# Performance work log

Hardware: AMD Instinct MI355X
Metric: run time of the kernel (lower is better)

## Reference

```python
import jax, jax.numpy as jnp
import numpy as np

B, CIN, H, W = 8, 64, 56, 56
COUT, K, HEADS, PAD = 64, 7, 8, 3


def hswish(x):
    return x * jnp.clip(x + 3.0, 0.0, 6.0) / 6.0


def grouped_1x1(x, w):
    # x: (B, Cin, H, W); w: (G, Cout_g, Cin_g)  -> (B, Cout, H, W)
    b, cin, h, wd = x.shape
    g = w.shape[0]
    xg = x.reshape(b, g, cin // g, h, wd)
    y = jnp.einsum('bgihw,goi->bgohw', xg, w)
    return y.reshape(b, g * w.shape[1], h, wd)


def unfold2d(x, k, h_out, w_out):
    # x: (B, C, Hp, Wp) -> (B, C, h_out, w_out, k, k), stride 1
    cols = [x[:, :, i:i + h_out, j:j + w_out] for i in range(k) for j in range(k)]
    s = jnp.stack(cols, axis=-1)  # (B,C,h,w,k*k) in (kh,kw) row-major order
    return s.reshape(*s.shape[:-1], k, k)


def setup_inputs() -> dict:
    key = jax.random.key(0)
    k1, k2, k3, k4, k5, k6 = jax.random.split(key, 6)
    cin_g, cout_g = CIN // HEADS, COUT // HEADS
    fan_out = cout_g  # 1x1 kernel, kaiming fan_out per group
    std = float(np.sqrt(2.0 / fan_out))
    return {
        'x': jax.random.normal(k1, (B, CIN, H, W), dtype=jnp.float32),
        'wq': jax.random.normal(k2, (HEADS, cout_g, cin_g), dtype=jnp.float32) * std,
        'wk': jax.random.normal(k3, (HEADS, cout_g, cin_g), dtype=jnp.float32) * std,
        'wv': jax.random.normal(k4, (HEADS, cout_g, cin_g), dtype=jnp.float32) * std,
        'rel_h': jax.random.normal(k5, (COUT // 2, 1, 1, K, 1), dtype=jnp.float32),
        'rel_w': jax.random.normal(k6, (COUT // 2, 1, 1, 1, K), dtype=jnp.float32),
    }


def reference(x, wq, wk, wv, rel_h, rel_w):
    b, _, h, w = x.shape
    heads = wq.shape[0]
    d = COUT // heads
    padded = jnp.pad(x, ((0, 0), (0, 0), (PAD, PAD), (PAD, PAD)))
    q = grouped_1x1(x, wq)                       # (B, Cout, H, W)
    k_full = grouped_1x1(padded, wk)             # (B, Cout, Hp, Wp)
    v_full = hswish(grouped_1x1(padded, wv))
    kp = unfold2d(k_full, K, h, w)               # (B, Cout, H, W, K, K)
    vp = unfold2d(v_full, K, h, w)
    kh, kw_ = kp[:, :COUT // 2], kp[:, COUT // 2:]
    kp = jnp.concatenate((kh + rel_h, kw_ + rel_w), axis=1)
    kp = kp.reshape(b, heads, d, h, w, K * K)
    vp = vp.reshape(b, heads, d, h, w, K * K)
    qh = q.reshape(b, heads, d, h, w, 1)
    # NOTE: faithful to original bug: sqrt(heads // out_channels) == 0.0
    scale = float(np.sqrt(heads // COUT))
    logits = (qh * kp).sum(axis=2, keepdims=True) * scale  # (B,heads,1,H,W,K*K)
    attn = jax.nn.softmax(logits, axis=-1)
    out = (attn * vp).sum(axis=-1)               # (B, heads, d, H, W)
    return out.reshape(b, heads * d, h, w)
```

## Files before the change

### kernel.cpp

```cpp
#include <hip/hip_runtime.h>


namespace {
constexpr int Bn = 8, CINn = 64, Hn = 56, Wn = 56;
constexpr int HEADSn = 8;
constexpr int PADn = 3;
constexpr int TH = 4;
constexpr int NTILES = Hn / TH;
constexpr int PH = TH + 6;
constexpr int PW = Wn + 6;
constexpr int RS = 80;
constexpr int THREADS = 256;
constexpr int NRUNS = Wn / 2;
}

__device__ __forceinline__ int sx(int x) { return x + (x >> 2); }
__device__ __forceinline__ float4 f4add(float4 a, float4 b) {
    return make_float4(a.x + b.x, a.y + b.y, a.z + b.z, a.w + b.w);
}
__device__ __forceinline__ float4 f4sub(float4 a, float4 b) {
    return make_float4(a.x - b.x, a.y - b.y, a.z - b.z, a.w - b.w);
}

__global__ __launch_bounds__(THREADS) void saconv_r2(
    const float* __restrict__ x, const float* __restrict__ wv,
    float* __restrict__ out)
{
    __shared__ float  wvs[64];
    __shared__ float4 vt[2 * PH * RS];
    __shared__ float4 vs[2 * TH * RS];

    const int bid  = blockIdx.x;
    const int tile = bid % NTILES;
    const int g    = (bid / NTILES) % HEADSn;
    const int b    = bid / (NTILES * HEADSn);
    const int h0   = tile * TH;
    const int tid  = threadIdx.x;

    if (tid < 64) wvs[tid] = wv[g * 64 + tid];
    __syncthreads();

    const float* __restrict__ xg = x + (size_t)(b * CINn + g * 8) * (Hn * Wn);

    for (int p = tid; p < PH * PW; p += THREADS) {
        const int py = p / PW;
        const int px = p - py * PW;
        const int y  = h0 + py - PADn;
        const int xx = px - PADn;
        float4 v0 = make_float4(0.f, 0.f, 0.f, 0.f);
        float4 v1 = v0;
        if ((unsigned)y < (unsigned)Hn && (unsigned)xx < (unsigned)Wn) {
            float in[8];
            #pragma unroll
            for (int i = 0; i < 8; ++i)
                in[i] = xg[i * (Hn * Wn) + y * Wn + xx];
            float a[8];
            #pragma unroll
            for (int o = 0; o < 8; ++o) {
                float s = 0.f;
                #pragma unroll
                for (int i = 0; i < 8; ++i)
                    s = fmaf(wvs[o * 8 + i], in[i], s);
                float t = fminf(fmaxf(s + 3.f, 0.f), 6.f);
                a[o] = s * t * (1.f / 6.f);
            }
            v0 = make_float4(a[0], a[1], a[2], a[3]);
            v1 = make_float4(a[4], a[5], a[6], a[7]);
        }
        vt[(0 * PH + py) * RS + sx(px)] = v0;
        vt[(1 * PH + py) * RS + sx(px)] = v1;
    }
    __syncthreads();

    if (tid < 2 * PW * 2) {
        const int g4 = tid & 1;
        const int r  = tid >> 1;
        const int xx = r % PW;
        const int yh = r / PW;
        const int y0 = 2 * yh;
        float4 rv[8];
        #pragma unroll
        for (int j = 0; j < 8; ++j)
            rv[j] = vt[(g4 * PH + y0 + j) * RS + sx(xx)];
        float4 s = rv[0];
        #pragma unroll
        for (int j = 1; j < 7; ++j) s = f4add(s, rv[j]);
        vs[(g4 * TH + y0) * RS + sx(xx)] = s;
        s = f4add(s, f4sub(rv[7], rv[0]));
        vs[(g4 * TH + y0 + 1) * RS + sx(xx)] = s;
    }
    __syncthreads();

    if (tid < TH * NRUNS * 2) {
        const int g4  = tid & 1;
        const int r   = tid >> 1;
        const int run = r % NRUNS;
        const int y   = r / NRUNS;
        const int x0  = run * 2;
        float4 rv[8];
        #pragma unroll
        for (int j = 0; j < 8; ++j)
            rv[j] = vs[(g4 * TH + y) * RS + sx(x0 + j)];
        float4 s0 = rv[0];
        #pragma unroll
        for (int j = 1; j < 7; ++j) s0 = f4add(s0, rv[j]);
        float4 s1 = f4add(s0, f4sub(rv[7], rv[0]));
        const float inv = 1.f / 49.f;
        float* ob = out + ((size_t)(b * CINn + g * 8 + g4 * 4) * Hn + (h0 + y)) * Wn + x0;
        const int plane = Hn * Wn;
        float2 st;
        st.x = s0.x * inv; st.y = s1.x * inv; *(float2*)(ob + 0 * plane) = st;
        st.x = s0.y * inv; st.y = s1.y * inv; *(float2*)(ob + 1 * plane) = st;
        st.x = s0.z * inv; st.y = s1.z * inv; *(float2*)(ob + 2 * plane) = st;
        st.x = s0.w * inv; st.y = s1.w * inv; *(float2*)(ob + 3 * plane) = st;
    }
}

extern "C" void kernel_launch(void* const* d_in, const int* in_sizes, int n_in,
                              void* d_out, int out_size, void* d_ws, size_t ws_size,
                              hipStream_t stream) {
    const float* x  = (const float*)d_in[0];
    const float* wv = (const float*)d_in[3];
    float* out = (float*)d_out;

    dim3 grid(Bn * HEADSn * NTILES);
    saconv_r2<<<grid, THREADS, 0, stream>>>(x, wv, out);
}
```

Measured before the change: 11.75 us.

## Fuse vertical box sum into register pass and halve tile height

Each thread now owns one padded column and one 4-channel half-head. It computes the hswish value projection for 8 input rows and accumulates the two vertical 7-row sums directly in registers, so the intermediate value tile in shared memory and one barrier stage go away. Weights are loaded into registers instead of shared memory. Tile height drops to 2 rows with 128 threads, which doubles the block count. The trade-off is more redundant recomputation and re-reading of input rows, since 8 rows are processed for every 2 output rows.

Result: slower. 13.30 us (+13.3%).

```diff
diff --git a/kernel.cpp b/kernel.cpp
--- a/kernel.cpp
+++ b/kernel.cpp
@@ -5,12 +5,11 @@
 constexpr int Bn = 8, CINn = 64, Hn = 56, Wn = 56;
 constexpr int HEADSn = 8;
 constexpr int PADn = 3;
-constexpr int TH = 4;
+constexpr int TH = 2;
 constexpr int NTILES = Hn / TH;
-constexpr int PH = TH + 6;
 constexpr int PW = Wn + 6;
-constexpr int RS = 80;
-constexpr int THREADS = 256;
+constexpr int RSH = 78;
+constexpr int THREADS = 128;
 constexpr int NRUNS = Wn / 2;
 }
 
@@ -22,13 +21,11 @@
     return make_float4(a.x - b.x, a.y - b.y, a.z - b.z, a.w - b.w);
 }
 
-__global__ __launch_bounds__(THREADS) void saconv_r2(
+__global__ __launch_bounds__(THREADS) void saconv_r4(
     const float* __restrict__ x, const float* __restrict__ wv,
     float* __restrict__ out)
 {
-    __shared__ float  wvs[64];
-    __shared__ float4 vt[2 * PH * RS];
-    __shared__ float4 vs[2 * TH * RS];
+    __shared__ float4 hs[2 * TH * RSH];
 
     const int bid  = blockIdx.x;
     const int tile = bid % NTILES;
@@ -37,82 +34,72 @@
     const int h0   = tile * TH;
     const int tid  = threadIdx.x;
 
-    if (tid < 64) wvs[tid] = wv[g * 64 + tid];
-    __syncthreads();
+    const int g4 = tid >> 6;
+    const int px = tid & 63;
+    const int xx = px - PADn;
+    const bool colok = (unsigned)xx < (unsigned)Wn;
+
+    const float* __restrict__ wg = wv + g * 64 + g4 * 32;
+    float w[32];
+    #pragma unroll
+    for (int i = 0; i < 32; ++i) w[i] = wg[i];
 
     const float* __restrict__ xg = x + (size_t)(b * CINn + g * 8) * (Hn * Wn);
 
-    for (int p = tid; p < PH * PW; p += THREADS) {
-        const int py = p / PW;
-        const int px = p - py * PW;
-        const int y  = h0 + py - PADn;
-        const int xx = px - PADn;
-        float4 v0 = make_float4(0.f, 0.f, 0.f, 0.f);
-        float4 v1 = v0;
-        if ((unsigned)y < (unsigned)Hn && (unsigned)xx < (unsigned)Wn) {
+    float4 s0 = make_float4(0.f, 0.f, 0.f, 0.f);
+    float4 s1 = s0;
+    #pragma unroll
+    for (int r = 0; r < 8; ++r) {
+        const int y = h0 + r - PADn;
+        float4 v = make_float4(0.f, 0.f, 0.f, 0.f);
+        if (colok && (unsigned)y < (unsigned)Hn) {
             float in[8];
             #pragma unroll
             for (int i = 0; i < 8; ++i)
                 in[i] = xg[i * (Hn * Wn) + y * Wn + xx];
-            float a[8];
+            float a[4];
             #pragma unroll
-            for (int o = 0; o < 8; ++o) {
+            for (int o = 0; o < 4; ++o) {
                 float s = 0.f;
                 #pragma unroll
                 for (int i = 0; i < 8; ++i)
-                    s = fmaf(wvs[o * 8 + i], in[i], s);
+                    s = fmaf(w[o * 8 + i], in[i], s);
                 float t = fminf(fmaxf(s + 3.f, 0.f), 6.f);
                 a[o] = s * t * (1.f / 6.f);
             }
-            v0 = make_float4(a[0], a[1], a[2], a[3]);
-            v1 = make_float4(a[4], a[5], a[6], a[7]);
+            v = make_float4(a[0], a[1], a[2], a[3]);
         }
-        vt[(0 * PH + py) * RS + sx(px)] = v0;
-        vt[(1 * PH + py) * RS + sx(px)] = v1;
+        if (r < 7) s0 = f4add(s0, v);
+        if (r >= 1) s1 = f4add(s1, v);
     }
-    __syncthreads();
-
-    if (tid < 2 * PW * 2) {
-        const int g4 = tid & 1;
-        const int r  = tid >> 1;
-        const int xx = r % PW;
-        const int yh = r / PW;
-        const int y0 = 2 * yh;
-        float4 rv[8];
-        #pragma unroll
-        for (int j = 0; j < 8; ++j)
-            rv[j] = vt[(g4 * PH + y0 + j) * RS + sx(xx)];
-        float4 s = rv[0];
-        #pragma unroll
-        for (int j = 1; j < 7; ++j) s = f4add(s, rv[j]);
-        vs[(g4 * TH + y0) * RS + sx(xx)] = s;
-        s = f4add(s, f4sub(rv[7], rv[0]));
-        vs[(g4 * TH + y0 + 1) * RS + sx(xx)] = s;
+    if (px < PW) {
+        hs[(g4 * TH + 0) * RSH + sx(px)] = s0;
+        hs[(g4 * TH + 1) * RSH + sx(px)] = s1;
     }
     __syncthreads();
 
     if (tid < TH * NRUNS * 2) {
-        const int g4  = tid & 1;
-        const int r   = tid >> 1;
-        const int run = r % NRUNS;
-        const int y   = r / NRUNS;
+        const int g4b = tid & 1;
+        const int rem = tid >> 1;
+        const int run = rem % NRUNS;
+        const int y   = rem / NRUNS;
         const int x0  = run * 2;
         float4 rv[8];
         #pragma unroll
         for (int j = 0; j < 8; ++j)
-            rv[j] = vs[(g4 * TH + y) * RS + sx(x0 + j)];
-        float4 s0 = rv[0];
+            rv[j] = hs[(g4b * TH + y) * RSH + sx(x0 + j)];
+        float4 t0 = rv[0];
         #pragma unroll
-        for (int j = 1; j < 7; ++j) s0 = f4add(s0, rv[j]);
-        float4 s1 = f4add(s0, f4sub(rv[7], rv[0]));
+        for (int j = 1; j < 7; ++j) t0 = f4add(t0, rv[j]);
+        float4 t1 = f4add(t0, f4sub(rv[7], rv[0]));
         const float inv = 1.f / 49.f;
-        float* ob = out + ((size_t)(b * CINn + g * 8 + g4 * 4) * Hn + (h0 + y)) * Wn + x0;
+        float* ob = out + ((size_t)(b * CINn + g * 8 + g4b * 4) * Hn + (h0 + y)) * Wn + x0;
         const int plane = Hn * Wn;
         float2 st;
-        st.x = s0.x * inv; st.y = s1.x * inv; *(float2*)(ob + 0 * plane) = st;
-        st.x = s0.y * inv; st.y = s1.y * inv; *(float2*)(ob + 1 * plane) = st;
-        st.x = s0.z * inv; st.y = s1.z * inv; *(float2*)(ob + 2 * plane) = st;
-        st.x = s0.w * inv; st.y = s1.w * inv; *(float2*)(ob + 3 * plane) = st;
+        st.x = t0.x * inv; st.y = t1.x * inv; *(float2*)(ob + 0 * plane) = st;
+        st.x = t0.y * inv; st.y = t1.y * inv; *(float2*)(ob + 1 * plane) = st;
+        st.x = t0.z * inv; st.y = t1.z * inv; *(float2*)(ob + 2 * plane) = st;
+        st.x = t0.w * inv; st.y = t1.w * inv; *(float2*)(ob + 3 * plane) = st;
     }
 }
 
@@ -124,5 +111,5 @@
     float* out = (float*)d_out;
 
     dim3 grid(Bn * HEADSn * NTILES);
-    saconv_r2<<<grid, THREADS, 0, stream>>>(x, wv, out);
+    saconv_r4<<<grid, THREADS, 0, stream>>>(x, wv, out);
 }
```
